# Kernel tuning notes

Measured on AMD Instinct MI355X. Metric: run time of the kernel, lower is better.

The kernel has to match this reference:

```python
import jax, jax.numpy as jnp
from jax import lax
import numpy as np

B, A, N_CLS = 2, 3, 3          # batch, anchors per voxel, classes
D, H, W = 64, 128, 128         # 3D feature-map volume
M = 128                        # padded max GT boxes per sample
ALPHA = 2.0                    # focal exponent (module's self.alpha)
EPS = 1e-4                     # probability clamp (module's self.eps)
NMS = True                     # max-pool NMS filtering on neg mask


def setup_inputs() -> dict:
    key = jax.random.key(0)
    logits = jax.random.normal(key, (B, N_CLS * A, D, H, W), dtype=jnp.float32)
    rng = np.random.default_rng(0)
    # prob_gt: -1 = hard negative to mine, 0 = ignore, c in [1..N_CLS] = positive of class c
    prob = np.zeros((B, A, D, H, W), np.float32)
    prob[rng.random((B, A, D, H, W)) < 0.3] = -1.0
    coord = -np.ones((B, M, 4), np.int64)  # rows (a,d,h,w), -1 padded
    k = 96  # valid GT boxes per sample
    for b in range(B):
        a = rng.integers(0, A, k)
        d = rng.integers(0, D, k)
        h = rng.integers(0, H, k)
        w = rng.integers(0, W, k)
        c = rng.integers(1, N_CLS + 1, k)
        prob[b, a, d, h, w] = c
        coord[b, :k] = np.stack([a, d, h, w], 1)
    return {
        "logits": logits,
        "prob_gt": jnp.asarray(prob),
        "coord_gt": jnp.asarray(coord),
        "weight_cls": jnp.ones((N_CLS,), jnp.float32),
    }


def _per_sample(pp, cg, pg, weight_cls):
    # pp: [N_CLS, A, D, H, W] probs; cg: [M,4] int coords (-1 padded); pg: [A,D,H,W]
    valid = cg[:, 0] > -1                              # [M]
    a = jnp.where(valid, cg[:, 0], 0)
    d = jnp.where(valid, cg[:, 1], 0)
    h = jnp.where(valid, cg[:, 2], 0)
    w = jnp.where(valid, cg[:, 3], 0)
    cls = jnp.where(valid, pg[a, d, h, w].astype(jnp.int32) - 1, 0)  # [M]
    vf = valid.astype(pp.dtype)
    # positive term
    pt = pp[cls, a, d, h, w]                           # [M]
    w_pos = lax.stop_gradient(1.0 - pt) ** ALPHA * weight_cls[cls] * vf
    l_pos = -jnp.sum(jnp.log(pt) * w_pos)
    c_pos = jnp.sum(w_pos)
    # "other classes at positive locations" term
    po = pp[:, a, d, h, w]                             # [N_CLS, M]
    w_oth = lax.stop_gradient(
        jnp.maximum(po - (pt - 0.1)[None, :], 0.0)
        * (po > 0.5) * (pt > 0.5)[None, :]
    )
    # torch `weight[cls_gt] = 0` zeroes whole rows for every gt class present
    zero_rows = jnp.any((jnp.arange(N_CLS)[:, None] == cls[None, :]) & valid[None, :], axis=1)
    w_oth = jnp.where(zero_rows[:, None], 0.0, w_oth) * vf[None, :]
    l_oth = jnp.sum(-jnp.log(1.0 - po) * w_oth)
    c_oth = jnp.sum(w_oth)
    return l_pos, c_pos, l_oth, c_oth


def _focal(logits, prob_gt, coord_gt, weight_cls):
    p = jnp.clip(jax.nn.sigmoid(logits), EPS, 1.0 - EPS)  # [B, N_CLS*A, D, H, W]
    bsz, C, dd, hh, ww = logits.shape
    negmask = (prob_gt == -1).astype(p.dtype)             # [B, A, D, H, W]
    negmask = jnp.repeat(negmask[:, None], N_CLS, axis=1).reshape(p.shape)
    if NMS:
        pooled = lax.reduce_window(logits, -jnp.inf, lax.max,
                                   (1, 1, 3, 3, 3), (1, 1, 1, 1, 1), 'SAME')
        max_filter = lax.stop_gradient((pooled == logits).astype(p.dtype))
        thresh_filter = (p > EPS).astype(p.dtype)
        negmask = negmask * max_filter * thresh_filter
    w_neg = lax.stop_gradient(p) ** ALPHA * negmask
    loss_neg = -jnp.sum(jnp.log(1.0 - p) * w_neg)
    count_neg = jnp.sum(w_neg)
    p6 = p.reshape(bsz, N_CLS, C // N_CLS, dd, hh, ww)
    l_pos, c_pos, l_oth, c_oth = jax.vmap(_per_sample, in_axes=(0, 0, 0, None))(
        p6, coord_gt, prob_gt, weight_cls)
    return jnp.stack([jnp.sum(l_pos), loss_neg, jnp.sum(l_oth),
                      jnp.sum(c_pos), count_neg, jnp.sum(c_oth)])


def reference(logits, prob_gt, coord_gt, weight_cls):
    # returns [cls_loss_pos, cls_loss_neg, cls_loss_other, count_pos, count_neg, count_other]
    return _focal(logits, prob_gt, coord_gt, weight_cls)
```

## Files before the change

### kernel.cpp

```cpp
#include <hip/hip_runtime.h>
#include <cstdint>
#include <cstddef>

#define B_    2
#define A_    3
#define NCLS_ 3
#define CH_   9
#define D_    64
#define H_    128
#define W_    128
#define M_    128
#define TD    16
#define EPS_      1e-4f
#define ONE_M_EPS 0.9999f
#define NLOG2E    -1.4426950408889634f
#define LN2_      0.6931471805599453f

__device__ __forceinline__ float4 fmax4(float4 a, float4 b) {
    return make_float4(fmaxf(a.x, b.x), fmaxf(a.y, b.y),
                       fmaxf(a.z, b.z), fmaxf(a.w, b.w));
}

__device__ __forceinline__ float exp2_fast(float x) { return __builtin_amdgcn_exp2f(x); }
__device__ __forceinline__ float log2_fast(float x) { return __builtin_amdgcn_logf(x); }

struct Raw { float4 c, e, pg; };

__global__ __launch_bounds__(256) void neg_kernel(
    const float* __restrict__ logits, const float* __restrict__ prob,
    float* __restrict__ partials)
{
    const int orig = blockIdx.x;
    const int swz  = (orig & 7) * 144 + (orig >> 3);
    const int tid  = threadIdx.x;
    const int lw   = tid & 31;
    const int lane = tid & 63;
    const int hwi  = tid >> 5;
    const int half = hwi & 1;
    const float NEG = -INFINITY;

    const int htile  = swz & 15;
    const int dchunk = (swz >> 4) & 3;
    const int bc     = swz >> 6;
    const int b = bc / CH_;
    const int a = (bc - b * CH_) % A_;
    const int d0 = dchunk * TD;
    const int r  = htile * 8 + hwi;
    const int er = half ? min(r + 1, H_ - 1) : max(r - 1, 0);

    const size_t HW = (size_t)H_ * W_;
    const float* Cb = logits + (size_t)bc * D_ * HW + (size_t)r  * W_ + 4 * lw;
    const float* Eb = logits + (size_t)bc * D_ * HW + (size_t)er * W_ + 4 * lw;
    const float* Pb = prob + (size_t)(b * A_ + a) * D_ * HW + (size_t)r * W_ + 4 * lw;

    auto ldc = [&](int dq) -> float4 {
        const int dc = min(max(dq, 0), D_ - 1);
        return *(const float4*)(Cb + (size_t)dc * HW);
    };
    auto lde = [&](int dq) -> float4 {
        const int dc = min(max(dq, 0), D_ - 1);
        return *(const float4*)(Eb + (size_t)dc * HW);
    };
    auto ldpg = [&](int dq) -> float4 {
        const int dc = min(max(dq, 0), D_ - 1);
        return *(const float4*)(Pb + (size_t)dc * HW);
    };
    auto shfl4 = [&](float4 v) -> float4 {
        const int p = lane ^ 32;
        return make_float4(__shfl(v.x, p, 64), __shfl(v.y, p, 64),
                           __shfl(v.z, p, 64), __shfl(v.w, p, 64));
    };
    auto hv = [&](const Raw& rw) -> float4 {
        return fmax4(rw.c, fmax4(rw.e, shfl4(rw.c)));
    };

    Raw rm1; rm1.c = ldc(d0 - 1); rm1.e = lde(d0 - 1);
    Raw r0;  r0.c  = ldc(d0);     r0.e  = lde(d0);     r0.pg  = ldpg(d0);
    Raw rawD; rawD.c = ldc(d0+1); rawD.e = lde(d0+1);  rawD.pg = ldpg(d0+1);
    Raw rawE; rawE.c = ldc(d0+2); rawE.e = lde(d0+2);  rawE.pg = ldpg(d0+2);

    float4 hwmA = hv(rm1);
    float4 hwmB = hv(r0);
    float4 xc   = r0.c;
    float4 pgc  = r0.pg;

    float lacc2 = 0.0f, cacc = 0.0f;

    #pragma unroll
    for (int j = 0; j < TD; ++j) {
        Raw rawN = rawE;
        if (j <= TD - 3) {
            rawN.c = ldc(d0 + j + 3); rawN.e = lde(d0 + j + 3);
            rawN.pg = ldpg(d0 + j + 3);
        }

        const float4 hwmC = hv(rawD);
        const float4 xN   = rawD.c;
        const float4 pgN  = rawD.pg;

        float4 cm = fmax4(hwmA, fmax4(hwmB, hwmC));
        const float lftv = __shfl(cm.w, (lane + 63) & 63, 64);
        const float rgtv = __shfl(cm.x, (lane + 1) & 63, 64);
        const float left  = (lw == 0)  ? NEG : lftv;
        const float right = (lw == 31) ? NEG : rgtv;
        float4 m;
        m.x = fmaxf(left, fmaxf(cm.x, cm.y));
        m.y = fmaxf(cm.x, fmaxf(cm.y, cm.z));
        m.z = fmaxf(cm.y, fmaxf(cm.z, cm.w));
        m.w = fmaxf(cm.z, fmaxf(cm.w, right));

        {
            const float x = xc.x;
            const bool pre = (pgc.x == -1.0f) & (m.x == x);
            if (__any(pre)) {
                const float u = exp2_fast(x * NLOG2E);
                const float p = __builtin_amdgcn_fmed3f(
                                    __builtin_amdgcn_rcpf(1.0f + u), EPS_, ONE_M_EPS);
                const float wn = (pre & (p > EPS_)) ? p * p : 0.0f;
                cacc += wn;
                lacc2 = fmaf(log2_fast(1.0f - p), wn, lacc2);
            }
        }
        {
            const float x = xc.y;
            const bool pre = (pgc.y == -1.0f) & (m.y == x);
            if (__any(pre)) {
                const float u = exp2_fast(x * NLOG2E);
                const float p = __builtin_amdgcn_fmed3f(
                                    __builtin_amdgcn_rcpf(1.0f + u), EPS_, ONE_M_EPS);
                const float wn = (pre & (p > EPS_)) ? p * p : 0.0f;
                cacc += wn;
                lacc2 = fmaf(log2_fast(1.0f - p), wn, lacc2);
            }
        }
        {
            const float x = xc.z;
            const bool pre = (pgc.z == -1.0f) & (m.z == x);
            if (__any(pre)) {
                const float u = exp2_fast(x * NLOG2E);
                const float p = __builtin_amdgcn_fmed3f(
                                    __builtin_amdgcn_rcpf(1.0f + u), EPS_, ONE_M_EPS);
                const float wn = (pre & (p > EPS_)) ? p * p : 0.0f;
                cacc += wn;
                lacc2 = fmaf(log2_fast(1.0f - p), wn, lacc2);
            }
        }
        {
            const float x = xc.w;
            const bool pre = (pgc.w == -1.0f) & (m.w == x);
            if (__any(pre)) {
                const float u = exp2_fast(x * NLOG2E);
                const float p = __builtin_amdgcn_fmed3f(
                                    __builtin_amdgcn_rcpf(1.0f + u), EPS_, ONE_M_EPS);
                const float wn = (pre & (p > EPS_)) ? p * p : 0.0f;
                cacc += wn;
                lacc2 = fmaf(log2_fast(1.0f - p), wn, lacc2);
            }
        }

        hwmA = hwmB; hwmB = hwmC;
        xc = xN; pgc = pgN;
        rawD = rawE; rawE = rawN;
    }

    float lacc = lacc2 * (-LN2_);

    #pragma unroll
    for (int off = 32; off > 0; off >>= 1) {
        lacc += __shfl_down(lacc, off);
        cacc += __shfl_down(cacc, off);
    }
    __shared__ float rl[4], rc[4];
    const int wv = threadIdx.x >> 6;
    if (lane == 0) { rl[wv] = lacc; rc[wv] = cacc; }
    __syncthreads();
    if (threadIdx.x == 0) {
        partials[2 * (size_t)blockIdx.x]     = rl[0] + rl[1] + rl[2] + rl[3];
        partials[2 * (size_t)blockIdx.x + 1] = rc[0] + rc[1] + rc[2] + rc[3];
    }
}

__global__ __launch_bounds__(256) void pos_reduce_kernel(
    const float* __restrict__ logits, const float* __restrict__ prob,
    const int* __restrict__ coord, const float* __restrict__ wcls,
    const float* __restrict__ partials, int nb, float* __restrict__ out)
{
    const int tid = threadIdx.x;
    const int b = tid >> 7;
    const int m = tid & (M_ - 1);
    __shared__ int zr[B_][NCLS_];
    if (tid < B_ * NCLS_) zr[tid / NCLS_][tid % NCLS_] = 0;
    __syncthreads();

    const int* cg = coord + ((size_t)b * M_ + m) * 4;
    const int c0 = cg[0];
    const bool valid = c0 > -1;
    const int a = valid ? c0    : 0;
    const int d = valid ? cg[1] : 0;
    const int h = valid ? cg[2] : 0;
    const int w = valid ? cg[3] : 0;

    const size_t HW = (size_t)H_ * W_;
    const size_t sp = (size_t)d * HW + (size_t)h * W_ + w;

    const float pv = prob[((size_t)b * A_ + a) * D_ * HW + sp];
    const int cls = valid ? ((int)pv - 1) : 0;
    if (valid) zr[b][cls] = 1;
    __syncthreads();

    auto sigclip = [](float x) {
        float p = 1.0f / (1.0f + __expf(-x));
        return fminf(fmaxf(p, EPS_), ONE_M_EPS);
    };

    const float vf = valid ? 1.0f : 0.0f;
    const float pt = sigclip(logits[((size_t)(b * CH_ + cls * A_ + a)) * D_ * HW + sp]);
    const float wp = (1.0f - pt) * (1.0f - pt) * wcls[cls] * vf;
    float lpos = -__logf(pt) * wp;
    float cpos = wp;

    float loth = 0.0f, coth = 0.0f;
    const bool ptg = pt > 0.5f;
    #pragma unroll
    for (int cc = 0; cc < NCLS_; ++cc) {
        const float po = sigclip(logits[((size_t)(b * CH_ + cc * A_ + a)) * D_ * HW + sp]);
        float wo = fmaxf(po - (pt - 0.1f), 0.0f);
        wo = (po > 0.5f && ptg) ? wo : 0.0f;
        wo = zr[b][cc] ? 0.0f : wo;
        wo *= vf;
        loth -= __logf(1.0f - po) * wo;
        coth += wo;
    }

    float l = 0.0f, c = 0.0f;
    for (int i = tid; i < nb; i += 256) {
        l += partials[2 * (size_t)i];
        c += partials[2 * (size_t)i + 1];
    }

    #pragma unroll
    for (int off = 32; off > 0; off >>= 1) {
        lpos += __shfl_down(lpos, off);
        cpos += __shfl_down(cpos, off);
        loth += __shfl_down(loth, off);
        coth += __shfl_down(coth, off);
        l    += __shfl_down(l, off);
        c    += __shfl_down(c, off);
    }
    __shared__ float r6[4][6];
    const int lane = tid & 63, wv = tid >> 6;
    if (lane == 0) {
        r6[wv][0] = lpos; r6[wv][1] = cpos; r6[wv][2] = loth;
        r6[wv][3] = coth; r6[wv][4] = l;    r6[wv][5] = c;
    }
    __syncthreads();
    if (tid == 0) {
        out[0] = r6[0][0] + r6[1][0] + r6[2][0] + r6[3][0];
        out[3] = r6[0][1] + r6[1][1] + r6[2][1] + r6[3][1];
        out[2] = r6[0][2] + r6[1][2] + r6[2][2] + r6[3][2];
        out[5] = r6[0][3] + r6[1][3] + r6[2][3] + r6[3][3];
        out[1] = r6[0][4] + r6[1][4] + r6[2][4] + r6[3][4];
        out[4] = r6[0][5] + r6[1][5] + r6[2][5] + r6[3][5];
    }
}

extern "C" void kernel_launch(void* const* d_in, const int* in_sizes, int n_in,
                              void* d_out, int out_size, void* d_ws, size_t ws_size,
                              hipStream_t stream)
{
    const float* logits = (const float*)d_in[0];
    const float* prob   = (const float*)d_in[1];
    const int*   coord  = (const int*)d_in[2];
    const float* wcls   = (const float*)d_in[3];
    float* out = (float*)d_out;

    const int nb = B_ * CH_ * (H_ / 8) * (D_ / TD);

    float* partials = (float*)d_ws;

    neg_kernel<<<dim3(nb), dim3(256), 0, stream>>>(logits, prob, partials);
    pos_reduce_kernel<<<dim3(1), dim3(256), 0, stream>>>(logits, prob, coord, wcls,
                                                         partials, nb, out);
}
```

Before: 138.6 us.

## Process two H rows per half-wave and reorder blocks so classes share prob tiles

Each half-wave now handles two adjacent H rows instead of one, so each H tile covers 16 rows and only one extra halo row is loaded per pair. This cuts the redundant halo loads in the 3x3x3 max filter. The D chunk shrinks to 8 and block indexing is reordered so the three class channels for the same anchor run as neighbouring blocks, which should improve L2 reuse of the prob tile. The cost is more registers per thread and a larger relative D halo, since each 8-deep chunk still loads two extra slices.

```diff
diff --git a/kernel.cpp b/kernel.cpp
--- a/kernel.cpp
+++ b/kernel.cpp
@@ -10,7 +10,8 @@
 #define H_    128
 #define W_    128
 #define M_    128
-#define TD    16
+#define TD    8
+#define THT   16
 #define EPS_      1e-4f
 #define ONE_M_EPS 0.9999f
 #define NLOG2E    -1.4426950408889634f
@@ -24,7 +25,7 @@
 __device__ __forceinline__ float exp2_fast(float x) { return __builtin_amdgcn_exp2f(x); }
 __device__ __forceinline__ float log2_fast(float x) { return __builtin_amdgcn_logf(x); }
 
-struct Raw { float4 c, e, pg; };
+struct Raw { float4 c0, c1, e, p0, p1; };
 
 __global__ __launch_bounds__(256) void neg_kernel(
     const float* __restrict__ logits, const float* __restrict__ prob,
@@ -36,69 +37,55 @@
     const int lw   = tid & 31;
     const int lane = tid & 63;
     const int hwi  = tid >> 5;
-    const int half = hwi & 1;
+    const bool evenh = (hwi & 1) == 0;
     const float NEG = -INFINITY;
 
-    const int htile  = swz & 15;
-    const int dchunk = (swz >> 4) & 3;
-    const int bc     = swz >> 6;
-    const int b = bc / CH_;
-    const int a = (bc - b * CH_) % A_;
+    const int htile  = swz & 7;
+    const int u      = swz >> 3;
+    const int cls    = u % 3;
+    const int v      = u / 3;
+    const int dchunk = v & 7;
+    const int g      = v >> 3;
+    const int b = g / 3, a = g - 3 * b;
+    const int bc = b * CH_ + cls * A_ + a;
     const int d0 = dchunk * TD;
-    const int r  = htile * 8 + hwi;
-    const int er = half ? min(r + 1, H_ - 1) : max(r - 1, 0);
+    const int R0 = htile * THT + 2 * hwi;
+    const int er = evenh ? max(R0 - 1, 0) : min(R0 + 2, H_ - 1);
 
     const size_t HW = (size_t)H_ * W_;
-    const float* Cb = logits + (size_t)bc * D_ * HW + (size_t)r  * W_ + 4 * lw;
-    const float* Eb = logits + (size_t)bc * D_ * HW + (size_t)er * W_ + 4 * lw;
-    const float* Pb = prob + (size_t)(b * A_ + a) * D_ * HW + (size_t)r * W_ + 4 * lw;
-
-    auto ldc = [&](int dq) -> float4 {
+    const float* Lc = logits + (size_t)bc * D_ * HW + 4 * lw;
+    const float* Pp = prob + (size_t)(b * A_ + a) * D_ * HW + 4 * lw;
+    const float* C0 = Lc + (size_t)R0 * W_;
+    const float* C1 = Lc + (size_t)(R0 + 1) * W_;
+    const float* Eb = Lc + (size_t)er * W_;
+    const float* P0 = Pp + (size_t)R0 * W_;
+    const float* P1 = Pp + (size_t)(R0 + 1) * W_;
+
+    auto ld = [&](const float* base, int dq) -> float4 {
         const int dc = min(max(dq, 0), D_ - 1);
-        return *(const float4*)(Cb + (size_t)dc * HW);
-    };
-    auto lde = [&](int dq) -> float4 {
-        const int dc = min(max(dq, 0), D_ - 1);
-        return *(const float4*)(Eb + (size_t)dc * HW);
-    };
-    auto ldpg = [&](int dq) -> float4 {
-        const int dc = min(max(dq, 0), D_ - 1);
-        return *(const float4*)(Pb + (size_t)dc * HW);
-    };
-    auto shfl4 = [&](float4 v) -> float4 {
+        return *(const float4*)(base + (size_t)dc * HW);
+    };
+    auto ldraw = [&](int dq) -> Raw {
+        Raw r;
+        r.c0 = ld(C0, dq); r.c1 = ld(C1, dq); r.e = ld(Eb, dq);
+        r.p0 = ld(P0, dq); r.p1 = ld(P1, dq);
+        return r;
+    };
+    auto shfl4 = [&](float4 vv) -> float4 {
         const int p = lane ^ 32;
-        return make_float4(__shfl(v.x, p, 64), __shfl(v.y, p, 64),
-                           __shfl(v.z, p, 64), __shfl(v.w, p, 64));
-    };
-    auto hv = [&](const Raw& rw) -> float4 {
-        return fmax4(rw.c, fmax4(rw.e, shfl4(rw.c)));
-    };
-
-    Raw rm1; rm1.c = ldc(d0 - 1); rm1.e = lde(d0 - 1);
-    Raw r0;  r0.c  = ldc(d0);     r0.e  = lde(d0);     r0.pg  = ldpg(d0);
-    Raw rawD; rawD.c = ldc(d0+1); rawD.e = lde(d0+1);  rawD.pg = ldpg(d0+1);
-    Raw rawE; rawE.c = ldc(d0+2); rawE.e = lde(d0+2);  rawE.pg = ldpg(d0+2);
-
-    float4 hwmA = hv(rm1);
-    float4 hwmB = hv(r0);
-    float4 xc   = r0.c;
-    float4 pgc  = r0.pg;
-
-    float lacc2 = 0.0f, cacc = 0.0f;
-
-    #pragma unroll
-    for (int j = 0; j < TD; ++j) {
-        Raw rawN = rawE;
-        if (j <= TD - 3) {
-            rawN.c = ldc(d0 + j + 3); rawN.e = lde(d0 + j + 3);
-            rawN.pg = ldpg(d0 + j + 3);
-        }
-
-        const float4 hwmC = hv(rawD);
-        const float4 xN   = rawD.c;
-        const float4 pgN  = rawD.pg;
-
-        float4 cm = fmax4(hwmA, fmax4(hwmB, hwmC));
+        return make_float4(__shfl(vv.x, p, 64), __shfl(vv.y, p, 64),
+                           __shfl(vv.z, p, 64), __shfl(vv.w, p, 64));
+    };
+    auto hv = [&](const Raw& rw, float4& vm0, float4& vm1) {
+        const float4 s0 = shfl4(rw.c0);
+        const float4 s1 = shfl4(rw.c1);
+        const float4 nlo = evenh ? rw.e : s1;
+        const float4 nhi = evenh ? s0 : rw.e;
+        const float4 cc = fmax4(rw.c0, rw.c1);
+        vm0 = fmax4(nlo, cc);
+        vm1 = fmax4(cc, nhi);
+    };
+    auto wmax = [&](float4 cm) -> float4 {
         const float lftv = __shfl(cm.w, (lane + 63) & 63, 64);
         const float rgtv = __shfl(cm.x, (lane + 1) & 63, 64);
         const float left  = (lw == 0)  ? NEG : lftv;
@@ -108,58 +95,58 @@
         m.y = fmaxf(cm.x, fmaxf(cm.y, cm.z));
         m.z = fmaxf(cm.y, fmaxf(cm.z, cm.w));
         m.w = fmaxf(cm.z, fmaxf(cm.w, right));
-
-        {
-            const float x = xc.x;
-            const bool pre = (pgc.x == -1.0f) & (m.x == x);
-            if (__any(pre)) {
-                const float u = exp2_fast(x * NLOG2E);
-                const float p = __builtin_amdgcn_fmed3f(
-                                    __builtin_amdgcn_rcpf(1.0f + u), EPS_, ONE_M_EPS);
-                const float wn = (pre & (p > EPS_)) ? p * p : 0.0f;
-                cacc += wn;
-                lacc2 = fmaf(log2_fast(1.0f - p), wn, lacc2);
-            }
+        return m;
+    };
+
+    float lacc2 = 0.0f, cacc = 0.0f;
+    auto epi = [&](float x, float pgv, float mv) {
+        const bool pre = (pgv == -1.0f) & (mv == x);
+        if (__any(pre)) {
+            const float uu = exp2_fast(x * NLOG2E);
+            const float p = __builtin_amdgcn_fmed3f(
+                                __builtin_amdgcn_rcpf(1.0f + uu), EPS_, ONE_M_EPS);
+            const float wn = (pre & (p > EPS_)) ? p * p : 0.0f;
+            cacc += wn;
+            lacc2 = fmaf(log2_fast(1.0f - p), wn, lacc2);
         }
-        {
-            const float x = xc.y;
-            const bool pre = (pgc.y == -1.0f) & (m.y == x);
-            if (__any(pre)) {
-                const float u = exp2_fast(x * NLOG2E);
-                const float p = __builtin_amdgcn_fmed3f(
-                                    __builtin_amdgcn_rcpf(1.0f + u), EPS_, ONE_M_EPS);
-                const float wn = (pre & (p > EPS_)) ? p * p : 0.0f;
-                cacc += wn;
-                lacc2 = fmaf(log2_fast(1.0f - p), wn, lacc2);
-            }
-        }
-        {
-            const float x = xc.z;
-            const bool pre = (pgc.z == -1.0f) & (m.z == x);
-            if (__any(pre)) {
-                const float u = exp2_fast(x * NLOG2E);
-                const float p = __builtin_amdgcn_fmed3f(
-                                    __builtin_amdgcn_rcpf(1.0f + u), EPS_, ONE_M_EPS);
-                const float wn = (pre & (p > EPS_)) ? p * p : 0.0f;
-                cacc += wn;
-                lacc2 = fmaf(log2_fast(1.0f - p), wn, lacc2);
-            }
-        }
-        {
-            const float x = xc.w;
-            const bool pre = (pgc.w == -1.0f) & (m.w == x);
-            if (__any(pre)) {
-                const float u = exp2_fast(x * NLOG2E);
-                const float p = __builtin_amdgcn_fmed3f(
-                                    __builtin_amdgcn_rcpf(1.0f + u), EPS_, ONE_M_EPS);
-                const float wn = (pre & (p > EPS_)) ? p * p : 0.0f;
-                cacc += wn;
-                lacc2 = fmaf(log2_fast(1.0f - p), wn, lacc2);
-            }
-        }
-
-        hwmA = hwmB; hwmB = hwmC;
-        xc = xN; pgc = pgN;
+    };
+
+    const float4 am1c0 = ld(C0, d0 - 1);
+    const float4 am1c1 = ld(C1, d0 - 1);
+    const float4 am1e  = ld(Eb, d0 - 1);
+    Raw r0   = ldraw(d0);
+    Raw rawD = ldraw(d0 + 1);
+    Raw rawE = ldraw(d0 + 2);
+
+    float4 vmA0, vmA1, vmB0, vmB1;
+    {
+        Raw rm1; rm1.c0 = am1c0; rm1.c1 = am1c1; rm1.e = am1e;
+        hv(rm1, vmA0, vmA1);
+    }
+    hv(r0, vmB0, vmB1);
+    float4 xc0 = r0.c0, xc1 = r0.c1, pgc0 = r0.p0, pgc1 = r0.p1;
+
+    #pragma unroll
+    for (int j = 0; j < TD; ++j) {
+        Raw rawN;
+        if (j <= TD - 3) rawN = ldraw(d0 + j + 3);
+        else             rawN = rawE;
+
+        float4 vmC0, vmC1;
+        hv(rawD, vmC0, vmC1);
+        const float4 xN0 = rawD.c0, xN1 = rawD.c1;
+        const float4 pN0 = rawD.p0, pN1 = rawD.p1;
+
+        const float4 m0 = wmax(fmax4(vmA0, fmax4(vmB0, vmC0)));
+        const float4 m1 = wmax(fmax4(vmA1, fmax4(vmB1, vmC1)));
+
+        epi(xc0.x, pgc0.x, m0.x); epi(xc0.y, pgc0.y, m0.y);
+        epi(xc0.z, pgc0.z, m0.z); epi(xc0.w, pgc0.w, m0.w);
+        epi(xc1.x, pgc1.x, m1.x); epi(xc1.y, pgc1.y, m1.y);
+        epi(xc1.z, pgc1.z, m1.z); epi(xc1.w, pgc1.w, m1.w);
+
+        vmA0 = vmB0; vmA1 = vmB1; vmB0 = vmC0; vmB1 = vmC1;
+        xc0 = xN0; xc1 = xN1; pgc0 = pN0; pgc1 = pN1;
         rawD = rawE; rawE = rawN;
     }
 
@@ -274,8 +261,7 @@
     const float* wcls   = (const float*)d_in[3];
     float* out = (float*)d_out;
 
-    const int nb = B_ * CH_ * (H_ / 8) * (D_ / TD);
-
+    const int nb = B_ * A_ * NCLS_ * (D_ / TD) * (H_ / THT);
     float* partials = (float*)d_ws;
 
     neg_kernel<<<dim3(nb), dim3(256), 0, stream>>>(logits, prob, partials);
```

Result: no change. 139.8 us (+0.8%).
